# Optimization experiments

Hardware: AMD Instinct MI355X
Metric: run time of the kernel (lower is better)

The kernel has to match this reference:

```python
import jax, jax.numpy as jnp
import numpy as np

TAU = 1.0

def setup_inputs() -> dict:
    key = jax.random.key(0)
    scores = jax.random.normal(key, (16, 2048), dtype=jnp.float32)
    return {"scores": scores}

def reference(scores):
    # scores: [B, n]
    B, n = scores.shape
    # row-sum of pairwise abs differences: Asum[b,i] = sum_k |s_i - s_k|
    Asum = jnp.sum(jnp.abs(scores[:, :, None] - scores[:, None, :]), axis=-1)  # [B, n]
    # scaling[j] = n + 1 - 2*(j+1)
    scaling = (n + 1 - 2 * (jnp.arange(n, dtype=jnp.float32) + 1.0))  # [n]
    # P_max[b, j, i] = s[b,i] * scaling[j] - Asum[b,i]
    P_max = scores[:, None, :] * scaling[None, :, None] - Asum[:, None, :]  # [B, n, n]
    P_hat = jax.nn.softmax(P_max / TAU, axis=-1)
    return P_hat
```

## Files before the change

### kernel.cpp

```cpp
#include <hip/hip_runtime.h>
#include <hip/hip_bf16.h>

#define N 2048
#define B 16

__global__ __launch_bounds__(256) void asum_kernel(const float* __restrict__ s,
                                                   float* __restrict__ asum) {
    const int b = blockIdx.y;
    const int i = blockIdx.x * 256 + threadIdx.x;

    __shared__ float row[N];
    for (int k = threadIdx.x; k < N; k += 256)
        row[k] = s[b * N + k];
    __syncthreads();

    const float si = row[i];
    float acc = 0.0f;
#pragma unroll 8
    for (int k = 0; k < N; ++k)
        acc += fabsf(si - row[k]);

    asum[b * N + i] = acc;
}

__global__ __launch_bounds__(256) void softmax_rows(const float* __restrict__ s,
                                                    const float* __restrict__ asum,
                                                    float* __restrict__ out) {
    const int j = blockIdx.x;
    const int b = blockIdx.y;
    const int t = threadIdx.x;
    const int lane = t & 63;
    const int wave = t >> 6;

    const float cj = (float)(N - 1 - 2 * j);

    const float4* s4 = (const float4*)(s + (size_t)b * N);
    const float4* a4 = (const float4*)(asum + (size_t)b * N);

    float4 sv0 = s4[t];
    float4 sv1 = s4[t + 256];
    float4 av0 = a4[t];
    float4 av1 = a4[t + 256];

    float v[8];
    v[0] = sv0.x * cj - av0.x;
    v[1] = sv0.y * cj - av0.y;
    v[2] = sv0.z * cj - av0.z;
    v[3] = sv0.w * cj - av0.w;
    v[4] = sv1.x * cj - av1.x;
    v[5] = sv1.y * cj - av1.y;
    v[6] = sv1.z * cj - av1.z;
    v[7] = sv1.w * cj - av1.w;

    float m = v[0];
#pragma unroll
    for (int i = 1; i < 8; ++i) m = fmaxf(m, v[i]);
#pragma unroll
    for (int off = 32; off >= 1; off >>= 1)
        m = fmaxf(m, __shfl_xor(m, off));

    __shared__ float redm[4];
    __shared__ float reds[4];
    if (lane == 0) redm[wave] = m;
    __syncthreads();
    m = fmaxf(fmaxf(redm[0], redm[1]), fmaxf(redm[2], redm[3]));

    float e[8];
    float sum = 0.0f;
#pragma unroll
    for (int i = 0; i < 8; ++i) {
        e[i] = __expf(v[i] - m);
        sum += e[i];
    }
#pragma unroll
    for (int off = 32; off >= 1; off >>= 1)
        sum += __shfl_xor(sum, off);
    if (lane == 0) reds[wave] = sum;
    __syncthreads();
    sum = (reds[0] + reds[1]) + (reds[2] + reds[3]);

    const float r = 1.0f / sum;

    float4 o0, o1;
    o0.x = e[0] * r; o0.y = e[1] * r; o0.z = e[2] * r; o0.w = e[3] * r;
    o1.x = e[4] * r; o1.y = e[5] * r; o1.z = e[6] * r; o1.w = e[7] * r;

    float4* o4 = (float4*)(out + ((size_t)b * N + j) * N);
    o4[t]       = o0;
    o4[t + 256] = o1;
}

extern "C" void kernel_launch(void* const* d_in, const int* in_sizes, int n_in,
                              void* d_out, int out_size, void* d_ws, size_t ws_size,
                              hipStream_t stream) {
    const float* scores = (const float*)d_in[0];
    float* out = (float*)d_out;
    float* asum = (float*)d_ws;

    dim3 g1(N / 256, B);
    asum_kernel<<<g1, 256, 0, stream>>>(scores, asum);

    dim3 g2(N, B);
    softmax_rows<<<g2, 256, 0, stream>>>(scores, asum, out);
}
```

Before: 278.9 us.

## Map one softmax row per wavefront, use nontemporal stores, vectorize asum loads

The softmax kernel now gives each 64-lane wave a whole output row, so each block handles four rows and the shared-memory reductions and __syncthreads barriers are gone. Each lane holds 32 values in registers, and output writes use nontemporal stores to avoid polluting the cache with the 256MB output. The asum kernel loads and reads shared memory as 4-wide vectors. The per-thread register count goes up, and the input row is re-read by every wave.

```diff
diff --git a/kernel.cpp b/kernel.cpp
--- a/kernel.cpp
+++ b/kernel.cpp
@@ -3,6 +3,8 @@
 
 #define N 2048
 #define B 16
+
+typedef float v4f __attribute__((ext_vector_type(4)));
 
 __global__ __launch_bounds__(256) void asum_kernel(const float* __restrict__ s,
                                                    float* __restrict__ asum) {
@@ -10,84 +12,78 @@
     const int i = blockIdx.x * 256 + threadIdx.x;
 
     __shared__ float row[N];
-    for (int k = threadIdx.x; k < N; k += 256)
-        row[k] = s[b * N + k];
+    const v4f* g4 = (const v4f*)(s + b * N);
+    v4f* r4 = (v4f*)row;
+    r4[threadIdx.x] = g4[threadIdx.x];
+    r4[threadIdx.x + 256] = g4[threadIdx.x + 256];
     __syncthreads();
 
     const float si = row[i];
+    const v4f* row4 = (const v4f*)row;
     float acc = 0.0f;
-#pragma unroll 8
-    for (int k = 0; k < N; ++k)
-        acc += fabsf(si - row[k]);
-
+#pragma unroll 4
+    for (int k = 0; k < N / 4; ++k) {
+        v4f rv = row4[k];
+        acc += fabsf(si - rv.x) + fabsf(si - rv.y) +
+               fabsf(si - rv.z) + fabsf(si - rv.w);
+    }
     asum[b * N + i] = acc;
 }
 
 __global__ __launch_bounds__(256) void softmax_rows(const float* __restrict__ s,
                                                     const float* __restrict__ asum,
                                                     float* __restrict__ out) {
-    const int j = blockIdx.x;
-    const int b = blockIdx.y;
     const int t = threadIdx.x;
     const int lane = t & 63;
     const int wave = t >> 6;
+    const int j = blockIdx.x * 4 + wave;
+    const int b = blockIdx.y;
 
     const float cj = (float)(N - 1 - 2 * j);
 
-    const float4* s4 = (const float4*)(s + (size_t)b * N);
-    const float4* a4 = (const float4*)(asum + (size_t)b * N);
+    const v4f* s4 = (const v4f*)(s + (size_t)b * N);
+    const v4f* a4 = (const v4f*)(asum + (size_t)b * N);
 
-    float4 sv0 = s4[t];
-    float4 sv1 = s4[t + 256];
-    float4 av0 = a4[t];
-    float4 av1 = a4[t + 256];
-
-    float v[8];
-    v[0] = sv0.x * cj - av0.x;
-    v[1] = sv0.y * cj - av0.y;
-    v[2] = sv0.z * cj - av0.z;
-    v[3] = sv0.w * cj - av0.w;
-    v[4] = sv1.x * cj - av1.x;
-    v[5] = sv1.y * cj - av1.y;
-    v[6] = sv1.z * cj - av1.z;
-    v[7] = sv1.w * cj - av1.w;
+    float v[32];
+#pragma unroll
+    for (int c = 0; c < 8; ++c) {
+        v4f sv = s4[c * 64 + lane];
+        v4f av = a4[c * 64 + lane];
+        v[c * 4 + 0] = sv.x * cj - av.x;
+        v[c * 4 + 1] = sv.y * cj - av.y;
+        v[c * 4 + 2] = sv.z * cj - av.z;
+        v[c * 4 + 3] = sv.w * cj - av.w;
+    }
 
     float m = v[0];
 #pragma unroll
-    for (int i = 1; i < 8; ++i) m = fmaxf(m, v[i]);
+    for (int i = 1; i < 32; ++i) m = fmaxf(m, v[i]);
 #pragma unroll
     for (int off = 32; off >= 1; off >>= 1)
         m = fmaxf(m, __shfl_xor(m, off));
 
-    __shared__ float redm[4];
-    __shared__ float reds[4];
-    if (lane == 0) redm[wave] = m;
-    __syncthreads();
-    m = fmaxf(fmaxf(redm[0], redm[1]), fmaxf(redm[2], redm[3]));
-
-    float e[8];
     float sum = 0.0f;
 #pragma unroll
-    for (int i = 0; i < 8; ++i) {
-        e[i] = __expf(v[i] - m);
-        sum += e[i];
+    for (int i = 0; i < 32; ++i) {
+        v[i] = __expf(v[i] - m);
+        sum += v[i];
     }
 #pragma unroll
     for (int off = 32; off >= 1; off >>= 1)
         sum += __shfl_xor(sum, off);
-    if (lane == 0) reds[wave] = sum;
-    __syncthreads();
-    sum = (reds[0] + reds[1]) + (reds[2] + reds[3]);
 
     const float r = 1.0f / sum;
 
-    float4 o0, o1;
-    o0.x = e[0] * r; o0.y = e[1] * r; o0.z = e[2] * r; o0.w = e[3] * r;
-    o1.x = e[4] * r; o1.y = e[5] * r; o1.z = e[6] * r; o1.w = e[7] * r;
-
-    float4* o4 = (float4*)(out + ((size_t)b * N + j) * N);
-    o4[t]       = o0;
-    o4[t + 256] = o1;
+    v4f* o4 = (v4f*)(out + ((size_t)b * N + j) * N);
+#pragma unroll
+    for (int c = 0; c < 8; ++c) {
+        v4f o;
+        o.x = v[c * 4 + 0] * r;
+        o.y = v[c * 4 + 1] * r;
+        o.z = v[c * 4 + 2] * r;
+        o.w = v[c * 4 + 3] * r;
+        __builtin_nontemporal_store(o, &o4[c * 64 + lane]);
+    }
 }
 
 extern "C" void kernel_launch(void* const* d_in, const int* in_sizes, int n_in,
@@ -100,6 +96,6 @@
     dim3 g1(N / 256, B);
     asum_kernel<<<g1, 256, 0, stream>>>(scores, asum);
 
-    dim3 g2(N, B);
+    dim3 g2(N / 4, B);
     softmax_rows<<<g2, 256, 0, stream>>>(scores, asum, out);
 }
```

Result: no change. 279.2 us (+0.1%).
